# Kernel optimization log

Measured on AMD Instinct MI355X. Metric: run time of the kernel, lower is better.

The kernel has to match this reference:

```python
import jax, jax.numpy as jnp
import numpy as np


def quantize_ternary(w):
    # BitNet b1.58 absmean ternary quantization: clip(round(w/gamma), -1, 1) * gamma
    gamma = jnp.mean(jnp.abs(w)) + 1e-8
    return jnp.clip(jnp.round(w / gamma), -1.0, 1.0) * gamma


def setup_inputs() -> dict:
    key = jax.random.key(0)
    k1, k2, k3, k4, k5 = jax.random.split(key, 5)
    B, T, E, D, H = 8, 2048, 8, 128, 512
    x = jax.random.normal(k1, (B, T, E, D), dtype=jnp.float32)
    expert_weights = jax.random.uniform(k2, (B, T, E), dtype=jnp.float32)
    # nn.init.uniform_(-1, 1)
    gate_weights = jax.random.uniform(k3, (E, H, D), dtype=jnp.float32, minval=-1.0, maxval=1.0)
    up_weights = jax.random.uniform(k4, (E, H, D), dtype=jnp.float32, minval=-1.0, maxval=1.0)
    down_weights = jax.random.uniform(k5, (E, D, H), dtype=jnp.float32, minval=-1.0, maxval=1.0)
    return {"x": x, "expert_weights": expert_weights, "gate_weights": gate_weights,
            "up_weights": up_weights, "down_weights": down_weights}


def reference(x, expert_weights, gate_weights, up_weights, down_weights):
    # Ternary-quantize all expert weights (dynamic absmean scale per tensor)
    gate_w = quantize_ternary(gate_weights)  # [E, H, D]
    up_w = quantize_ternary(up_weights)      # [E, H, D]
    down_w = quantize_ternary(down_weights)  # [E, D, H]

    gate_out = jnp.einsum('bted,ehd->bteh', x, gate_w)
    up_out = jnp.einsum('bted,ehd->bteh', x, up_w)
    hidden = jax.nn.silu(gate_out) * up_out          # SwiGLU gating
    output = jnp.einsum('bteh,edh->bted', hidden, down_w)
    return output * expert_weights[..., None]        # routing-weighted outputs
```

## Files before the change

### kernel.cpp

```cpp
#include <hip/hip_runtime.h>

typedef __attribute__((ext_vector_type(8)))  __bf16 bf16x8;
typedef __attribute__((ext_vector_type(16))) float  f32x16;

struct U4 { unsigned int x, y, z, w; };

static __device__ __forceinline__ unsigned short f2bf(float f){
  unsigned int u = __builtin_bit_cast(unsigned int, f);
  u += 0x7fffu + ((u >> 16) & 1u);
  return (unsigned short)(u >> 16);
}

static __device__ __forceinline__ unsigned pk2(float lo, float hi){
  return (unsigned)f2bf(lo) | ((unsigned)f2bf(hi) << 16);
}

static __device__ __forceinline__ bf16x8 ldfrag(const void* p){
  U4 v = *(const U4*)p;
  return __builtin_bit_cast(bf16x8, v);
}

static __device__ __forceinline__ f32x16 mfma32(bf16x8 a, bf16x8 b, f32x16 c){
  return __builtin_amdgcn_mfma_f32_32x32x16_bf16(a, b, c, 0, 0, 0);
}

static __device__ __forceinline__ f32x16 zero16(){
  f32x16 z;
#pragma unroll
  for (int i = 0; i < 16; ++i) z[i] = 0.0f;
  return z;
}

static __device__ __forceinline__ void swap32(unsigned &a, unsigned &b){
  unsigned sa = (unsigned)__shfl_xor((int)a, 32, 64);
  unsigned sb = (unsigned)__shfl_xor((int)b, 32, 64);
  int l = (int)(threadIdx.x & 63);
  unsigned na = (l < 32) ? a : sb;
  unsigned nb = (l < 32) ? sa : b;
  a = na; b = nb;
}

#define IMG_EC  49152

__global__ void k_gamma(const float* __restrict__ gw, const float* __restrict__ uw,
                        const float* __restrict__ dw, float* __restrict__ sums){
  int t = blockIdx.y;
  const float* w = (t == 0) ? gw : (t == 1 ? uw : dw);
  int base = blockIdx.x * 2048 + threadIdx.x * 8;
  float4 a = *(const float4*)(w + base);
  float4 b = *(const float4*)(w + base + 4);
  float s = fabsf(a.x)+fabsf(a.y)+fabsf(a.z)+fabsf(a.w)
          + fabsf(b.x)+fabsf(b.y)+fabsf(b.z)+fabsf(b.w);
#pragma unroll
  for (int o = 32; o; o >>= 1) s += __shfl_xor(s, o);
  if ((threadIdx.x & 63) == 0) atomicAdd(&sums[t], s);
}

__global__ void k_quant(const float* __restrict__ gw, const float* __restrict__ uw,
                        const float* __restrict__ dw, const float* __restrict__ sums,
                        unsigned char* __restrict__ img){
  int b  = blockIdx.x;
  int tt = b % 3;
  int c  = (b / 3) & 7;
  int e  = b / 24;
  const float* w = (tt == 0) ? gw : (tt == 1 ? uw : dw);
  float inv = 1.0f / (sums[tt] * (1.0f / 524288.0f) + 1e-8f);
  unsigned char* dst = img + (size_t)(e * 8 + c) * IMG_EC + tt * 16384;
#pragma unroll
  for (int i = 0; i < 4; ++i){
    int grp = threadIdx.x + i * 256;
    int L = grp & 63, blkid = grp >> 6;
    int srcoff;
    if (tt < 2){
      int ht = blkid >> 3, ks = blkid & 7;
      int h  = c * 64 + ht * 32 + (L & 31);
      int dd = ks * 16 + (L >> 5) * 8;
      srcoff = (e * 512 + h) * 128 + dd;
    } else {
      int dt = blkid >> 2, ksp = blkid & 3;
      int d0 = dt * 32 + (L & 31);
      int h  = c * 64 + ksp * 16 + (L >> 5) * 8;
      srcoff = (e * 128 + d0) * 512 + h;
    }
    float4 f0 = *(const float4*)(w + srcoff);
    float4 f1 = *(const float4*)(w + srcoff + 4);
    float v[8] = {f0.x,f0.y,f0.z,f0.w,f1.x,f1.y,f1.z,f1.w};
    unsigned int o[4];
#pragma unroll
    for (int j = 0; j < 4; ++j){
      float q0 = fminf(1.0f, fmaxf(-1.0f, rintf(v[2*j]   * inv)));
      float q1 = fminf(1.0f, fmaxf(-1.0f, rintf(v[2*j+1] * inv)));
      o[j] = (unsigned int)f2bf(q0) | ((unsigned int)f2bf(q1) << 16);
    }
    *(U4*)(dst + grp * 16) = U4{o[0], o[1], o[2], o[3]};
  }
}

__global__ __launch_bounds__(512, 2) void k_moe(
    const float* __restrict__ x, const float* __restrict__ ew,
    const float* __restrict__ sums, const unsigned char* __restrict__ img,
    float* __restrict__ out){
  __shared__ char WB[49152];
  const int tile = blockIdx.x;
  const int e    = blockIdx.y;
  const int tid  = threadIdx.x;
  const int lane = tid & 63;
  const int wid  = tid >> 6;
  const int col  = lane & 31;
  const int hi   = lane >> 5;
  const int token = tile * 256 + wid * 32 + col;

  const float gg  = sums[0] * (1.0f/524288.0f) + 1e-8f;
  const float gu  = sums[1] * (1.0f/524288.0f) + 1e-8f;
  const float gdn = sums[2] * (1.0f/524288.0f) + 1e-8f;
  const float osc = gdn * ew[token * 8 + e];

  const float* xrow = x + ((size_t)token * 8 + e) * 128 + hi * 8;
  bf16x8 xf[8];
#pragma unroll
  for (int ks = 0; ks < 8; ++ks){
    float4 f0 = *(const float4*)(xrow + ks * 16);
    float4 f1 = *(const float4*)(xrow + ks * 16 + 4);
    U4 u{pk2(f0.x,f0.y), pk2(f0.z,f0.w), pk2(f1.x,f1.y), pk2(f1.z,f1.w)};
    xf[ks] = __builtin_bit_cast(bf16x8, u);
  }

  f32x16 O0 = zero16(), O1 = zero16(), O2 = zero16(), O3 = zero16();

  const unsigned char* wsrc0 = img + (size_t)e * 8 * IMG_EC;

  U4 stg[6];
#pragma unroll
  for (int i = 0; i < 6; ++i)
    stg[i] = *(const U4*)(wsrc0 + (size_t)(tid + i * 512) * 16);

  for (int c = 0; c < 8; ++c){
    if (c) __syncthreads();
#pragma unroll
    for (int i = 0; i < 6; ++i)
      *(U4*)(WB + (tid + i * 512) * 16) = stg[i];
    __syncthreads();

    if (c < 7){
      const unsigned char* wsrc = wsrc0 + (size_t)(c + 1) * IMG_EC;
#pragma unroll
      for (int i = 0; i < 6; ++i)
        stg[i] = *(const U4*)(wsrc + (size_t)(tid + i * 512) * 16);
    }

    f32x16 Cg0 = zero16(), Cg1 = zero16(), Cu0 = zero16(), Cu1 = zero16();
#pragma unroll
    for (int ks = 0; ks < 8; ++ks){
      bf16x8 ag0 = ldfrag(WB +         ((0 * 8 + ks) * 64 + lane) * 16);
      bf16x8 ag1 = ldfrag(WB +         ((1 * 8 + ks) * 64 + lane) * 16);
      bf16x8 au0 = ldfrag(WB + 16384 + ((0 * 8 + ks) * 64 + lane) * 16);
      bf16x8 au1 = ldfrag(WB + 16384 + ((1 * 8 + ks) * 64 + lane) * 16);
      Cg0 = mfma32(ag0, xf[ks], Cg0);
      Cg1 = mfma32(ag1, xf[ks], Cg1);
      Cu0 = mfma32(au0, xf[ks], Cu0);
      Cu1 = mfma32(au1, xf[ks], Cu1);
    }

    bf16x8 hf[4];
#pragma unroll
    for (int ht = 0; ht < 2; ++ht){
      const f32x16& G = ht ? Cg1 : Cg0;
      const f32x16& U = ht ? Cu1 : Cu0;
#pragma unroll
      for (int s = 0; s < 2; ++s){
        float h[8];
#pragma unroll
        for (int j = 0; j < 8; ++j){
          float gv = G[s * 8 + j] * gg;
          float uv = U[s * 8 + j] * gu;
          h[j] = (gv / (1.0f + __expf(-gv))) * uv;
        }
        unsigned w0 = pk2(h[0], h[1]);
        unsigned w1 = pk2(h[2], h[3]);
        unsigned w2 = pk2(h[4], h[5]);
        unsigned w3 = pk2(h[6], h[7]);
        swap32(w0, w2);
        swap32(w1, w3);
        U4 u{w0, w1, w2, w3};
        hf[ht * 2 + s] = __builtin_bit_cast(bf16x8, u);
      }
    }

#pragma unroll
    for (int ks2 = 0; ks2 < 4; ++ks2){
      bf16x8 d0 = ldfrag(WB + 32768 + ((0 * 4 + ks2) * 64 + lane) * 16);
      bf16x8 d1 = ldfrag(WB + 32768 + ((1 * 4 + ks2) * 64 + lane) * 16);
      bf16x8 d2 = ldfrag(WB + 32768 + ((2 * 4 + ks2) * 64 + lane) * 16);
      bf16x8 d3 = ldfrag(WB + 32768 + ((3 * 4 + ks2) * 64 + lane) * 16);
      O0 = mfma32(d0, hf[ks2], O0);
      O1 = mfma32(d1, hf[ks2], O1);
      O2 = mfma32(d2, hf[ks2], O2);
      O3 = mfma32(d3, hf[ks2], O3);
    }
  }

  float* orow = out + ((size_t)token * 8 + e) * 128 + hi * 4;
#pragma unroll
  for (int dt = 0; dt < 4; ++dt){
    const f32x16& O = dt == 0 ? O0 : dt == 1 ? O1 : dt == 2 ? O2 : O3;
#pragma unroll
    for (int q = 0; q < 4; ++q){
      float4 v{O[q*4+0]*osc, O[q*4+1]*osc, O[q*4+2]*osc, O[q*4+3]*osc};
      *(float4*)(orow + dt * 32 + q * 8) = v;
    }
  }
}

extern "C" void kernel_launch(void* const* d_in, const int* in_sizes, int n_in,
                              void* d_out, int out_size, void* d_ws, size_t ws_size,
                              hipStream_t stream){
  const float* x  = (const float*)d_in[0];
  const float* ew = (const float*)d_in[1];
  const float* gw = (const float*)d_in[2];
  const float* uw = (const float*)d_in[3];
  const float* dw = (const float*)d_in[4];
  float* out = (float*)d_out;

  float* sums = (float*)d_ws;
  unsigned char* img = (unsigned char*)d_ws + 256;

  hipMemsetAsync(d_ws, 0, 16, stream);
  k_gamma<<<dim3(256, 3), 256, 0, stream>>>(gw, uw, dw, sums);
  k_quant<<<dim3(192), 256, 0, stream>>>(gw, uw, dw, sums, img);
  k_moe<<<dim3(64, 8), 512, 0, stream>>>(x, ew, sums, img, out);
}
```

Baseline: 179.8 us.

## Double-buffer expert weight chunks in LDS via direct global-to-LDS loads

Replaces register-staged weight prefetch with global_load_lds direct copies into a double-buffered 96KB dynamic LDS region, so each chunk's load overlaps compute on the previous one with a single barrier per iteration. It also computes gate/up in two halves to cut live accumulator registers, swaps the division for a hardware reciprocal, and sets waves-per-EU to 2. The change doubles LDS use per block, which may limit occupancy, and relies on the barrier ordering being correct for the async LDS writes.

```diff
diff --git a/kernel.cpp b/kernel.cpp
--- a/kernel.cpp
+++ b/kernel.cpp
@@ -29,6 +29,12 @@
 #pragma unroll
   for (int i = 0; i < 16; ++i) z[i] = 0.0f;
   return z;
+}
+
+static __device__ __forceinline__ void gload16(const void* g, void* l){
+  __builtin_amdgcn_global_load_lds(
+      (const __attribute__((address_space(1))) unsigned int*)g,
+      (__attribute__((address_space(3))) unsigned int*)l, 16, 0, 0);
 }
 
 static __device__ __forceinline__ void swap32(unsigned &a, unsigned &b){
@@ -96,11 +102,11 @@
   }
 }
 
-__global__ __launch_bounds__(512, 2) void k_moe(
-    const float* __restrict__ x, const float* __restrict__ ew,
-    const float* __restrict__ sums, const unsigned char* __restrict__ img,
-    float* __restrict__ out){
-  __shared__ char WB[49152];
+__global__ __attribute__((amdgpu_waves_per_eu(2, 2))) __launch_bounds__(512)
+void k_moe(const float* __restrict__ x, const float* __restrict__ ew,
+           const float* __restrict__ sums, const unsigned char* __restrict__ img,
+           float* __restrict__ out){
+  extern __shared__ char smem[];
   const int tile = blockIdx.x;
   const int e    = blockIdx.y;
   const int tid  = threadIdx.x;
@@ -113,7 +119,12 @@
   const float gg  = sums[0] * (1.0f/524288.0f) + 1e-8f;
   const float gu  = sums[1] * (1.0f/524288.0f) + 1e-8f;
   const float gdn = sums[2] * (1.0f/524288.0f) + 1e-8f;
-  const float osc = gdn * ew[token * 8 + e];
+
+  const unsigned char* wsrc0 = img + (size_t)e * 8 * IMG_EC;
+
+#pragma unroll
+  for (int i = 0; i < 6; ++i)
+    gload16(wsrc0 + (size_t)(tid + i * 512) * 16, smem + (tid + i * 512) * 16);
 
   const float* xrow = x + ((size_t)token * 8 + e) * 128 + hi * 8;
   bf16x8 xf[8];
@@ -127,53 +138,38 @@
 
   f32x16 O0 = zero16(), O1 = zero16(), O2 = zero16(), O3 = zero16();
 
-  const unsigned char* wsrc0 = img + (size_t)e * 8 * IMG_EC;
-
-  U4 stg[6];
-#pragma unroll
-  for (int i = 0; i < 6; ++i)
-    stg[i] = *(const U4*)(wsrc0 + (size_t)(tid + i * 512) * 16);
-
+  __syncthreads();
+
+#pragma unroll 2
   for (int c = 0; c < 8; ++c){
-    if (c) __syncthreads();
-#pragma unroll
-    for (int i = 0; i < 6; ++i)
-      *(U4*)(WB + (tid + i * 512) * 16) = stg[i];
-    __syncthreads();
-
+    const char* cur = smem + (c & 1) * 49152;
     if (c < 7){
       const unsigned char* wsrc = wsrc0 + (size_t)(c + 1) * IMG_EC;
+      char* nxt = smem + ((c + 1) & 1) * 49152;
 #pragma unroll
       for (int i = 0; i < 6; ++i)
-        stg[i] = *(const U4*)(wsrc + (size_t)(tid + i * 512) * 16);
-    }
-
-    f32x16 Cg0 = zero16(), Cg1 = zero16(), Cu0 = zero16(), Cu1 = zero16();
-#pragma unroll
-    for (int ks = 0; ks < 8; ++ks){
-      bf16x8 ag0 = ldfrag(WB +         ((0 * 8 + ks) * 64 + lane) * 16);
-      bf16x8 ag1 = ldfrag(WB +         ((1 * 8 + ks) * 64 + lane) * 16);
-      bf16x8 au0 = ldfrag(WB + 16384 + ((0 * 8 + ks) * 64 + lane) * 16);
-      bf16x8 au1 = ldfrag(WB + 16384 + ((1 * 8 + ks) * 64 + lane) * 16);
-      Cg0 = mfma32(ag0, xf[ks], Cg0);
-      Cg1 = mfma32(ag1, xf[ks], Cg1);
-      Cu0 = mfma32(au0, xf[ks], Cu0);
-      Cu1 = mfma32(au1, xf[ks], Cu1);
+        gload16(wsrc + (size_t)(tid + i * 512) * 16, nxt + (tid + i * 512) * 16);
     }
 
     bf16x8 hf[4];
 #pragma unroll
     for (int ht = 0; ht < 2; ++ht){
-      const f32x16& G = ht ? Cg1 : Cg0;
-      const f32x16& U = ht ? Cu1 : Cu0;
+      f32x16 Cg = zero16(), Cu = zero16();
+#pragma unroll
+      for (int ks = 0; ks < 8; ++ks){
+        bf16x8 ag = ldfrag(cur +         ((ht * 8 + ks) * 64 + lane) * 16);
+        bf16x8 au = ldfrag(cur + 16384 + ((ht * 8 + ks) * 64 + lane) * 16);
+        Cg = mfma32(ag, xf[ks], Cg);
+        Cu = mfma32(au, xf[ks], Cu);
+      }
 #pragma unroll
       for (int s = 0; s < 2; ++s){
         float h[8];
 #pragma unroll
         for (int j = 0; j < 8; ++j){
-          float gv = G[s * 8 + j] * gg;
-          float uv = U[s * 8 + j] * gu;
-          h[j] = (gv / (1.0f + __expf(-gv))) * uv;
+          float gv = Cg[s * 8 + j] * gg;
+          float uv = Cu[s * 8 + j] * gu;
+          h[j] = gv * __builtin_amdgcn_rcpf(1.0f + __expf(-gv)) * uv;
         }
         unsigned w0 = pk2(h[0], h[1]);
         unsigned w1 = pk2(h[2], h[3]);
@@ -188,17 +184,20 @@
 
 #pragma unroll
     for (int ks2 = 0; ks2 < 4; ++ks2){
-      bf16x8 d0 = ldfrag(WB + 32768 + ((0 * 4 + ks2) * 64 + lane) * 16);
-      bf16x8 d1 = ldfrag(WB + 32768 + ((1 * 4 + ks2) * 64 + lane) * 16);
-      bf16x8 d2 = ldfrag(WB + 32768 + ((2 * 4 + ks2) * 64 + lane) * 16);
-      bf16x8 d3 = ldfrag(WB + 32768 + ((3 * 4 + ks2) * 64 + lane) * 16);
+      bf16x8 d0 = ldfrag(cur + 32768 + ((0 * 4 + ks2) * 64 + lane) * 16);
+      bf16x8 d1 = ldfrag(cur + 32768 + ((1 * 4 + ks2) * 64 + lane) * 16);
+      bf16x8 d2 = ldfrag(cur + 32768 + ((2 * 4 + ks2) * 64 + lane) * 16);
+      bf16x8 d3 = ldfrag(cur + 32768 + ((3 * 4 + ks2) * 64 + lane) * 16);
       O0 = mfma32(d0, hf[ks2], O0);
       O1 = mfma32(d1, hf[ks2], O1);
       O2 = mfma32(d2, hf[ks2], O2);
       O3 = mfma32(d3, hf[ks2], O3);
     }
-  }
-
+
+    if (c < 7) __syncthreads();
+  }
+
+  const float osc = gdn * ew[token * 8 + e];
   float* orow = out + ((size_t)token * 8 + e) * 128 + hi * 4;
 #pragma unroll
   for (int dt = 0; dt < 4; ++dt){
@@ -227,5 +226,5 @@
   hipMemsetAsync(d_ws, 0, 16, stream);
   k_gamma<<<dim3(256, 3), 256, 0, stream>>>(gw, uw, dw, sums);
   k_quant<<<dim3(192), 256, 0, stream>>>(gw, uw, dw, sums, img);
-  k_moe<<<dim3(64, 8), 512, 0, stream>>>(x, ew, sums, img, out);
-}
+  k_moe<<<dim3(64, 8), 512, 98304, stream>>>(x, ew, sums, img, out);
+}
```

Measured after the change: 177.1 us. Within noise of the previous version (-1.5%).
